# Kernel tuning notes

Measured on AMD Instinct MI355X. Metric: run time of the kernel, lower is better.

The kernel has to match this reference:

```python
import jax, jax.numpy as jnp
import numpy as np

LATENT_DIM = 128
HIDDEN = 20
BATCH = 32768


def _lstm_cell(x, h, c, W_ih, W_hh, b_ih, b_hh):
    # torch.nn.LSTMCell: gates order (i, f, g, o)
    gates = x @ W_ih.T + b_ih + h @ W_hh.T + b_hh
    i, f, g, o = jnp.split(gates, 4, axis=1)
    c_new = jax.nn.sigmoid(f) * c + jax.nn.sigmoid(i) * jnp.tanh(g)
    h_new = jax.nn.sigmoid(o) * jnp.tanh(c_new)
    return h_new, c_new


def setup_inputs() -> dict:
    key = jax.random.key(0)
    ks = jax.random.split(key, 10)
    L, H = LATENT_DIM, HIDDEN

    def u(k, shape, fan):  # torch LSTMCell init: U(-1/sqrt(hidden), 1/sqrt(hidden))
        b = 1.0 / np.sqrt(fan)
        return jax.random.uniform(k, shape, jnp.float32, -b, b)

    return {
        "mu": jax.random.normal(ks[0], (BATCH, L), jnp.float32),
        "log_var": jax.random.normal(ks[1], (BATCH, L), jnp.float32),
        "W_ih1": u(ks[2], (4 * H, L - 1), H),
        "W_hh1": u(ks[3], (4 * H, H), H),
        "b_ih1": u(ks[4], (4 * H,), H),
        "b_hh1": u(ks[5], (4 * H,), H),
        "W_ih2": u(ks[6], (8, 2 * H), 2),
        "W_hh2": u(ks[7], (8, 2), 2),
        "b_ih2": u(ks[8], (8,), 2),
        "b_hh2": u(ks[9], (8,), 2),
    }


def reference(mu, log_var, W_ih1, W_hh1, b_ih1, b_hh1, W_ih2, W_hh2, b_ih2, b_hh2):
    # sample=False path (the module's default)
    B, L = mu.shape
    H = W_hh1.shape[1]
    dt = mu.dtype
    # fixed reparameterization noise: eps[0] for the first draw, eps[k] for step k
    eps = jax.random.normal(jax.random.key(42), (L, B), dt)

    first_input = eps[0] * jnp.exp(0.5 * log_var[:, 0]) + mu[:, 0]  # [B]
    inp0 = jnp.zeros((B, L - 1), dt).at[:, 0].set(first_input)
    cols = jnp.arange(L - 1)
    mu_trunc = mu[:, : L - 1]

    def step(carry, xs):
        h1, c1, h2, c2, inp = carry
        idx, eps_t = xs
        h1, c1 = _lstm_cell(inp, h1, c1, W_ih1, W_hh1, b_ih1, b_hh1)
        out1 = jax.nn.leaky_relu(jnp.concatenate([h1, c1], axis=1))  # slope 0.01
        h2, c2 = _lstm_cell(out1, h2, c2, W_ih2, W_hh2, b_ih2, b_hh2)
        mu_r, lv_r = h2[:, 0], h2[:, 1]
        samp = eps_t * jnp.exp(0.5 * lv_r) + mu_r
        # next input = mu[:, :idx+1] zero-padded to width L-1 (sample=False branch)
        new_inp = jnp.where(cols <= idx, mu_trunc, jnp.zeros((), dt))
        return (h1, c1, h2, c2, new_inp), (mu_r, lv_r, samp)

    z = lambda n: jnp.zeros((B, n), dt)
    carry0 = (z(H), z(H), z(2), z(2), inp0)
    _, (mus, lvs, smps) = jax.lax.scan(step, carry0, (jnp.arange(1, L), eps[1:]))

    mus_full = jnp.concatenate([jnp.zeros((B, 1), dt), mus.T], axis=1)   # [B, L]
    lvs_full = jnp.concatenate([jnp.ones((B, 1), dt), lvs.T], axis=1)    # [B, L]
    samples = jnp.concatenate([first_input[:, None], smps.T], axis=1)    # [B, L]
    return mus_full, lvs_full, samples
```

## Files before the change

### kernel.cpp

```cpp
#include <hip/hip_runtime.h>
#include <stdint.h>
#include <math.h>

#define BATCH 32768
#define LDIM 128
#define HID 20

#define WS_AW  0
#define WS_AU  1280
#define WS_WCD 1792
#define WS_TOTAL 11952


__device__ __forceinline__ void threefry2x32(uint32_t x0, uint32_t x1,
                                             uint32_t& o0, uint32_t& o1) {
  const uint32_t k0 = 0u, k1 = 42u;
  const uint32_t k2 = k0 ^ k1 ^ 0x1BD11BDAu;
  uint32_t v0 = x0 + k0, v1 = x1 + k1;
#define TF_R(r) { v0 += v1; v1 = (v1 << (r)) | (v1 >> (32 - (r))); v1 ^= v0; }
  TF_R(13) TF_R(15) TF_R(26) TF_R(6)
  v0 += k1; v1 += k2 + 1u;
  TF_R(17) TF_R(29) TF_R(16) TF_R(24)
  v0 += k2; v1 += k0 + 2u;
  TF_R(13) TF_R(15) TF_R(26) TF_R(6)
  v0 += k0; v1 += k1 + 3u;
  TF_R(17) TF_R(29) TF_R(16) TF_R(24)
  v0 += k1; v1 += k2 + 4u;
  TF_R(13) TF_R(15) TF_R(26) TF_R(6)
  v0 += k2; v1 += k0 + 5u;
#undef TF_R
  o0 = v0; o1 = v1;
}

__device__ __forceinline__ float erfinv_xla_f32(float x) {
  float t = __fmul_rn(x, x);
  float w = -(float)log1p(-(double)t);
  float p;
  if (w < 5.0f) {
    w = __fadd_rn(w, -2.5f);
    p = 2.81022636e-08f;
    p = __fadd_rn(__fmul_rn(p, w), 3.43273939e-07f);
    p = __fadd_rn(__fmul_rn(p, w), -3.5233877e-06f);
    p = __fadd_rn(__fmul_rn(p, w), -4.39150654e-06f);
    p = __fadd_rn(__fmul_rn(p, w), 0.00021858087f);
    p = __fadd_rn(__fmul_rn(p, w), -0.00125372503f);
    p = __fadd_rn(__fmul_rn(p, w), -0.00417768164f);
    p = __fadd_rn(__fmul_rn(p, w), 0.246640727f);
    p = __fadd_rn(__fmul_rn(p, w), 1.50140941f);
  } else {
    w = __fadd_rn(__fsqrt_rn(w), -3.0f);
    p = -0.000200214257f;
    p = __fadd_rn(__fmul_rn(p, w), 0.000100950558f);
    p = __fadd_rn(__fmul_rn(p, w), 0.00134934322f);
    p = __fadd_rn(__fmul_rn(p, w), -0.00367342844f);
    p = __fadd_rn(__fmul_rn(p, w), 0.00573950773f);
    p = __fadd_rn(__fmul_rn(p, w), -0.0076224613f);
    p = __fadd_rn(__fmul_rn(p, w), 0.00943887047f);
    p = __fadd_rn(__fmul_rn(p, w), 1.00167406f);
    p = __fadd_rn(__fmul_rn(p, w), 2.83297682f);
  }
  return __fmul_rn(p, x);
}

__device__ __forceinline__ float eps_val(int t, int b) {
  uint32_t n = (uint32_t)t * 32768u + (uint32_t)b;
  uint32_t o0, o1;
  threefry2x32(0u, n, o0, o1);
  uint32_t bits = o0 ^ o1;
  const float lo    = __uint_as_float(0xBF7FFFFFu);
  const float sqrt2 = __uint_as_float(0x3FB504F3u);
  float f = __fadd_rn(__uint_as_float((bits >> 9) | 0x3F800000u), -1.0f);
  float u = __fadd_rn(__fmul_rn(f, 2.0f), lo);
  u = fmaxf(u, lo);
  return __fmul_rn(sqrt2, erfinv_xla_f32(u));
}

__device__ __forceinline__ float fexp2(float x) { return __builtin_amdgcn_exp2f(x); }
__device__ __forceinline__ float frcp(float x)  { return __builtin_amdgcn_rcpf(x); }
__device__ __forceinline__ float fexp(float x)  { return fexp2(1.442695040888963f * x); }
__device__ __forceinline__ float sigm(float x)  { return frcp(1.0f + fexp2(-1.442695040888963f * x)); }
__device__ __forceinline__ float tanhx(float x) { return 1.0f - 2.0f * frcp(1.0f + fexp2(2.885390081777926f * x)); }

typedef _Float16 f16x8 __attribute__((ext_vector_type(8)));
typedef _Float16 f16x2 __attribute__((ext_vector_type(2)));
typedef float    f32x4 __attribute__((ext_vector_type(4)));

__device__ __forceinline__ uint32_t packh(float x, float y) {
  f16x2 p;
  p.x = (_Float16)x;
  p.y = (_Float16)y;
  return __builtin_bit_cast(uint32_t, p);
}

__global__ void repack_kernel(const float* __restrict__ W_ih1,
                              const float* __restrict__ W_hh1,
                              const float* __restrict__ W_ih2,
                              float* __restrict__ ws) {
  uint32_t* wsu = (uint32_t*)ws;
  const int stride = gridDim.x * blockDim.x;
  const int tid0 = blockIdx.x * blockDim.x + threadIdx.x;
  for (int idx = tid0; idx < 1280; idx += stride) {
    int q = idx & 3, l = (idx >> 2) & 63, m = idx >> 8;
    int rA = l & 15, koct = l >> 4;
    int ty = rA & 3, u = 4 * m + (rA >> 2);
    int k0 = koct * 8 + 2 * q, k1 = k0 + 1;
    float w0 = (k0 < 20) ? W_hh1[(ty * 20 + u) * 20 + k0] : 0.0f;
    float w1 = (k1 < 20) ? W_hh1[(ty * 20 + u) * 20 + k1] : 0.0f;
    wsu[WS_AW + idx] = packh(w0, w1);
  }
  for (int idx = tid0; idx < 512; idx += stride) {
    int q = idx & 3, l = (idx >> 2) & 63, ks = idx >> 8;
    int j = l & 15, koct = l >> 4;
    int kk0 = ks * 32 + koct * 8 + 2 * q, kk1 = kk0 + 1;
    float w0 = (j < 8 && kk0 < 40)
                   ? W_ih2[j * 40 + (kk0 & 1) * 20 + (kk0 >> 1)] : 0.0f;
    float w1 = (j < 8 && kk1 < 40)
                   ? W_ih2[j * 40 + (kk1 & 1) * 20 + (kk1 >> 1)] : 0.0f;
    wsu[WS_AU + idx] = packh(w0, w1);
  }
  for (int idx = tid0; idx < 10160; idx += stride) {
    int grow = idx % 80, col = idx / 80;
    int u = grow >> 2, ty = grow & 3;
    ws[WS_WCD + idx] = W_ih1[(ty * 20 + u) * 127 + col];
  }
}

__global__ __launch_bounds__(256, 1) void sampler_kernel(
    const float* __restrict__ mu, const float* __restrict__ log_var,
    const float* __restrict__ ws,
    const float* __restrict__ b_ih1, const float* __restrict__ b_hh1,
    const float* __restrict__ W_hh2,
    const float* __restrict__ b_ih2, const float* __restrict__ b_hh2,
    float* __restrict__ out) {
  __shared__ float WcL[10160];
  __shared__ __align__(16) _Float16 hsh[4][640];
  __shared__ __align__(16) _Float16 lsh[4][1152];

  const int tid  = threadIdx.x;
  const int lane = tid & 63;
  const int wvl  = __builtin_amdgcn_readfirstlane(tid >> 6);
  const int sub  = lane >> 4;
  const int el   = lane & 15;
  const int elem = blockIdx.x * 64 + wvl * 16 + el;

  for (int i = tid; i < 10160; i += 256) WcL[i] = ws[WS_WCD + i];
  {
    uint32_t* hz = (uint32_t*)&hsh[0][0];
    for (int i = tid; i < 1280; i += 256) hz[i] = 0u;
    uint32_t* lz = (uint32_t*)&lsh[0][0];
    for (int i = tid; i < 2304; i += 256) lz[i] = 0u;
  }

  const uint32_t* wsu = (const uint32_t*)ws;
  f16x8 aw[5], au0, au1;
#pragma unroll
  for (int m = 0; m < 5; ++m)
    aw[m] = *(const f16x8*)(wsu + WS_AW + (m * 64 + lane) * 4);
  au0 = *(const f16x8*)(wsu + WS_AU + lane * 4);
  au1 = *(const f16x8*)(wsu + WS_AU + (64 + lane) * 4);

  __syncthreads();

  _Float16* hrow = &hsh[wvl][el * 40];
  _Float16* lrow = &lsh[wvl][el * 72];

  const float* mrow = mu + (size_t)elem * LDIM;

  float wa[4], wb[4], bb2[4], Sc[4], Ac[4], Bc[4];
#pragma unroll
  for (int r = 0; r < 4; ++r) {
    const int j = (4 * sub + r) & 7;
    wa[r]  = W_hh2[2 * j];
    wb[r]  = W_hh2[2 * j + 1];
    bb2[r] = b_ih2[j] + b_hh2[j];
    const bool isT = (j == 4) || (j == 5);
    Sc[r] = isT ?  2.885390081777926f : -1.442695040888963f;
    Ac[r] = isT ?  1.0f : 0.0f;
    Bc[r] = isT ? -2.0f : 1.0f;
  }

  float eps0 = eps_val(0, elem);
  float m0 = mrow[0];
  float fi = fmaf(eps0, fexp(0.5f * log_var[(size_t)elem * LDIM]), m0);

  f32x4 acc[5];
#pragma unroll
  for (int m = 0; m < 5; ++m) {
    f32x4 w0 = *(const f32x4*)&WcL[16 * m + 4 * sub];
#pragma unroll
    for (int r = 0; r < 4; ++r) {
      const int grow = 16 * m + 4 * sub + r;
      const int g = (grow & 3) * 20 + (grow >> 2);
      acc[m][r] = fmaf(fi, w0[r], b_ih1[g] + b_hh1[g]);
    }
  }

  float cst[5];
#pragma unroll
  for (int m = 0; m < 5; ++m) cst[m] = 0.0f;
  float h2a = 0.0f, h2b = 0.0f, c2a = 0.0f, c2b = 0.0f;

  float* out_mu = out;
  float* out_lv = out + (size_t)BATCH * LDIM;
  float* out_sp = out + 2 * (size_t)BATCH * LDIM;
  const size_t rowoff = (size_t)elem * LDIM;
  if (sub == 0)      { out_mu[rowoff] = 0.0f; out_lv[rowoff] = 1.0f; }
  else if (sub == 1) { out_sp[rowoff] = fi; }

  const f32x4 z4 = {0.0f, 0.0f, 0.0f, 0.0f};
  float xm_pref = m0;
  float eps4 = 0.0f, eps_old = 0.0f;

  auto lstm2_finish = [&](f16x8 bl0, f16x8 bl1, float eps_t, int e) {
    f32x4 d2 = __builtin_amdgcn_mfma_f32_16x16x32_f16(au0, bl0, z4, 0, 0, 0);
    d2 = __builtin_amdgcn_mfma_f32_16x16x32_f16(au1, bl1, d2, 0, 0, 0);
    float act[4];
#pragma unroll
    for (int r = 0; r < 4; ++r) {
      float g  = fmaf(h2a, wa[r], fmaf(h2b, wb[r], bb2[r])) + d2[r];
      float rc = frcp(1.0f + fexp2(Sc[r] * g));
      act[r] = fmaf(Bc[r], rc, Ac[r]);
    }
    float x0 = __shfl_xor(act[0], 16, 64);
    float x1 = __shfl_xor(act[1], 16, 64);
    float x2 = __shfl_xor(act[2], 16, 64);
    float x3 = __shfl_xor(act[3], 16, 64);
    const bool s1 = (sub & 1);
    float i20 = s1 ? x0 : act[0], i21 = s1 ? x1 : act[1];
    float f20 = s1 ? x2 : act[2], f21 = s1 ? x3 : act[3];
    float t20 = s1 ? act[0] : x0, t21 = s1 ? act[1] : x1;
    float o20 = s1 ? act[2] : x2, o21 = s1 ? act[3] : x3;
    c2a = fmaf(f20, c2a, i20 * t20);
    c2b = fmaf(f21, c2b, i21 * t21);
    h2a = o20 * tanhx(c2a);
    h2b = o21 * tanhx(c2b);
    if (sub == 0) {
      out_mu[rowoff + e] = h2a;
      out_lv[rowoff + e] = h2b;
    } else if (sub == 1) {
      out_sp[rowoff + e] = fmaf(eps_t, fexp(0.5f * h2b), h2a);
    }
  };

  for (int t = 1; t < LDIM; ++t) {
    float xm = xm_pref;
    xm_pref = mrow[t];

    const bool refresh = ((t - 1) & 3) == 0;
    if (refresh) { eps_old = eps4; eps4 = eps_val(t + sub, elem); }

    f16x8 bl0, bl1;
    if (t >= 2) {
      bl0 = *(const f16x8*)&lrow[sub * 8];
      bl1 = *(const f16x8*)&lrow[32 + sub * 8];
    }

    if (t >= 2) {
      if (t == 2) {
        float d0 = m0 - fi;
#pragma unroll
        for (int m = 0; m < 5; ++m) {
          f32x4 w0 = *(const f32x4*)&WcL[16 * m + 4 * sub];
#pragma unroll
          for (int r = 0; r < 4; ++r) acc[m][r] = fmaf(d0, w0[r], acc[m][r]);
        }
      }
#pragma unroll
      for (int m = 0; m < 5; ++m) {
        f32x4 wc = *(const f32x4*)&WcL[(t - 1) * 80 + 16 * m + 4 * sub];
#pragma unroll
        for (int r = 0; r < 4; ++r) acc[m][r] = fmaf(xm, wc[r], acc[m][r]);
      }
    }

    if (t >= 2) {
      float src = refresh ? eps_old : eps4;
      float eps_t = __shfl(src, ((t - 2) & 3) * 16 + el, 64);
      lstm2_finish(bl0, bl1, eps_t, t - 1);
    }

    f16x8 bh = *(const f16x8*)&hrow[sub * 8];
    f32x4 d[5];
#pragma unroll
    for (int m = 0; m < 5; ++m)
      d[m] = __builtin_amdgcn_mfma_f32_16x16x32_f16(aw[m], bh, acc[m], 0, 0, 0);

#pragma unroll
    for (int m = 0; m < 5; ++m) {
      float ik = sigm(d[m][0]), fk = sigm(d[m][1]);
      float gk = tanhx(d[m][2]), ok = sigm(d[m][3]);
      float cn = fmaf(fk, cst[m], ik * gk);
      cst[m] = cn;
      float hk = ok * tanhx(cn);
      hrow[4 * m + sub] = (_Float16)hk;
      float lh = (hk >= 0.0f) ? hk : 0.01f * hk;
      float lc = (cn >= 0.0f) ? cn : 0.01f * cn;
      f16x2 p; p.x = (_Float16)lh; p.y = (_Float16)lc;
      ((f16x2*)lrow)[4 * m + sub] = p;
    }
  }

  {
    f16x8 bl0 = *(const f16x8*)&lrow[sub * 8];
    f16x8 bl1 = *(const f16x8*)&lrow[32 + sub * 8];
    float eps_t = eps_val(127, elem);
    lstm2_finish(bl0, bl1, eps_t, 127);
  }
}

extern "C" void kernel_launch(void* const* d_in, const int* in_sizes, int n_in,
                              void* d_out, int out_size, void* d_ws, size_t ws_size,
                              hipStream_t stream) {
  (void)in_sizes; (void)n_in; (void)ws_size; (void)out_size;
  const float* mu      = (const float*)d_in[0];
  const float* log_var = (const float*)d_in[1];
  const float* W_ih1   = (const float*)d_in[2];
  const float* W_hh1   = (const float*)d_in[3];
  const float* b_ih1   = (const float*)d_in[4];
  const float* b_hh1   = (const float*)d_in[5];
  const float* W_ih2   = (const float*)d_in[6];
  const float* W_hh2   = (const float*)d_in[7];
  const float* b_ih2   = (const float*)d_in[8];
  const float* b_hh2   = (const float*)d_in[9];
  float* out = (float*)d_out;
  float* ws  = (float*)d_ws;

  repack_kernel<<<dim3(8), dim3(256), 0, stream>>>(W_ih1, W_hh1, W_ih2, ws);
  dim3 grid(BATCH / 64), block(256);
  sampler_kernel<<<grid, block, 0, stream>>>(mu, log_var, ws, b_ih1, b_hh1,
                                             W_hh2, b_ih2, b_hh2, out);
}
```

Baseline: 312.2 us.

## Keep MFMA B-operands in registers by permuting weight K-layout, drop LDS round-trip

```diff
diff --git a/kernel.cpp b/kernel.cpp
--- a/kernel.cpp
+++ b/kernel.cpp
@@ -84,6 +84,7 @@
 typedef _Float16 f16x8 __attribute__((ext_vector_type(8)));
 typedef _Float16 f16x2 __attribute__((ext_vector_type(2)));
 typedef float    f32x4 __attribute__((ext_vector_type(4)));
+typedef uint32_t u32x4 __attribute__((ext_vector_type(4)));
 
 __device__ __forceinline__ uint32_t packh(float x, float y) {
   f16x2 p;
@@ -104,18 +105,20 @@
     int rA = l & 15, koct = l >> 4;
     int ty = rA & 3, u = 4 * m + (rA >> 2);
     int k0 = koct * 8 + 2 * q, k1 = k0 + 1;
-    float w0 = (k0 < 20) ? W_hh1[(ty * 20 + u) * 20 + k0] : 0.0f;
-    float w1 = (k1 < 20) ? W_hh1[(ty * 20 + u) * 20 + k1] : 0.0f;
+    int mm0 = k0 & 7, mm1 = k1 & 7;
+    float w0 = (mm0 < 5) ? W_hh1[(ty * 20 + u) * 20 + (4 * mm0 + koct)] : 0.0f;
+    float w1 = (mm1 < 5) ? W_hh1[(ty * 20 + u) * 20 + (4 * mm1 + koct)] : 0.0f;
     wsu[WS_AW + idx] = packh(w0, w1);
   }
   for (int idx = tid0; idx < 512; idx += stride) {
     int q = idx & 3, l = (idx >> 2) & 63, ks = idx >> 8;
     int j = l & 15, koct = l >> 4;
-    int kk0 = ks * 32 + koct * 8 + 2 * q, kk1 = kk0 + 1;
-    float w0 = (j < 8 && kk0 < 40)
-                   ? W_ih2[j * 40 + (kk0 & 1) * 20 + (kk0 >> 1)] : 0.0f;
-    float w1 = (j < 8 && kk1 < 40)
-                   ? W_ih2[j * 40 + (kk1 & 1) * 20 + (kk1 >> 1)] : 0.0f;
+    int qq0 = 2 * q, qq1 = 2 * q + 1;
+    int mr0 = ks * 4 + (qq0 >> 1), mr1 = ks * 4 + (qq1 >> 1);
+    float w0 = (j < 8 && mr0 < 5)
+                   ? W_ih2[j * 40 + (qq0 & 1) * 20 + (4 * mr0 + koct)] : 0.0f;
+    float w1 = (j < 8 && mr1 < 5)
+                   ? W_ih2[j * 40 + (qq1 & 1) * 20 + (4 * mr1 + koct)] : 0.0f;
     wsu[WS_AU + idx] = packh(w0, w1);
   }
   for (int idx = tid0; idx < 10160; idx += stride) {
@@ -133,23 +136,14 @@
     const float* __restrict__ b_ih2, const float* __restrict__ b_hh2,
     float* __restrict__ out) {
   __shared__ float WcL[10160];
-  __shared__ __align__(16) _Float16 hsh[4][640];
-  __shared__ __align__(16) _Float16 lsh[4][1152];
 
   const int tid  = threadIdx.x;
   const int lane = tid & 63;
-  const int wvl  = __builtin_amdgcn_readfirstlane(tid >> 6);
   const int sub  = lane >> 4;
   const int el   = lane & 15;
-  const int elem = blockIdx.x * 64 + wvl * 16 + el;
+  const int elem = blockIdx.x * 64 + (tid >> 6) * 16 + el;
 
   for (int i = tid; i < 10160; i += 256) WcL[i] = ws[WS_WCD + i];
-  {
-    uint32_t* hz = (uint32_t*)&hsh[0][0];
-    for (int i = tid; i < 1280; i += 256) hz[i] = 0u;
-    uint32_t* lz = (uint32_t*)&lsh[0][0];
-    for (int i = tid; i < 2304; i += 256) lz[i] = 0u;
-  }
 
   const uint32_t* wsu = (const uint32_t*)ws;
   f16x8 aw[5], au0, au1;
@@ -160,9 +154,6 @@
   au1 = *(const f16x8*)(wsu + WS_AU + (64 + lane) * 4);
 
   __syncthreads();
-
-  _Float16* hrow = &hsh[wvl][el * 40];
-  _Float16* lrow = &lsh[wvl][el * 72];
 
   const float* mrow = mu + (size_t)elem * LDIM;
 
@@ -208,6 +199,11 @@
   else if (sub == 1) { out_sp[rowoff] = fi; }
 
   const f32x4 z4 = {0.0f, 0.0f, 0.0f, 0.0f};
+  const u32x4 zu = {0u, 0u, 0u, 0u};
+  f16x8 bh  = __builtin_bit_cast(f16x8, zu);
+  f16x8 blA = __builtin_bit_cast(f16x8, zu);
+  f16x8 blB = __builtin_bit_cast(f16x8, zu);
+
   float xm_pref = m0;
   float eps4 = 0.0f, eps_old = 0.0f;
 
@@ -249,12 +245,6 @@
     const bool refresh = ((t - 1) & 3) == 0;
     if (refresh) { eps_old = eps4; eps4 = eps_val(t + sub, elem); }
 
-    f16x8 bl0, bl1;
-    if (t >= 2) {
-      bl0 = *(const f16x8*)&lrow[sub * 8];
-      bl1 = *(const f16x8*)&lrow[32 + sub * 8];
-    }
-
     if (t >= 2) {
       if (t == 2) {
         float d0 = m0 - fi;
@@ -276,35 +266,50 @@
     if (t >= 2) {
       float src = refresh ? eps_old : eps4;
       float eps_t = __shfl(src, ((t - 2) & 3) * 16 + el, 64);
-      lstm2_finish(bl0, bl1, eps_t, t - 1);
-    }
-
-    f16x8 bh = *(const f16x8*)&hrow[sub * 8];
+      lstm2_finish(blA, blB, eps_t, t - 1);
+    }
+
     f32x4 d[5];
 #pragma unroll
     for (int m = 0; m < 5; ++m)
       d[m] = __builtin_amdgcn_mfma_f32_16x16x32_f16(aw[m], bh, acc[m], 0, 0, 0);
 
+    float hk[5], lh[5], lc[5];
 #pragma unroll
     for (int m = 0; m < 5; ++m) {
       float ik = sigm(d[m][0]), fk = sigm(d[m][1]);
       float gk = tanhx(d[m][2]), ok = sigm(d[m][3]);
       float cn = fmaf(fk, cst[m], ik * gk);
       cst[m] = cn;
-      float hk = ok * tanhx(cn);
-      hrow[4 * m + sub] = (_Float16)hk;
-      float lh = (hk >= 0.0f) ? hk : 0.01f * hk;
-      float lc = (cn >= 0.0f) ? cn : 0.01f * cn;
-      f16x2 p; p.x = (_Float16)lh; p.y = (_Float16)lc;
-      ((f16x2*)lrow)[4 * m + sub] = p;
+      float h1 = ok * tanhx(cn);
+      hk[m] = h1;
+      lh[m] = (h1 >= 0.0f) ? h1 : 0.01f * h1;
+      lc[m] = (cn >= 0.0f) ? cn : 0.01f * cn;
+    }
+
+    {
+      u32x4 tb;
+      tb.x = packh(hk[0], hk[1]);
+      tb.y = packh(hk[2], hk[3]);
+      tb.z = packh(hk[4], 0.0f);
+      tb.w = 0u;
+      bh = __builtin_bit_cast(f16x8, tb);
+      u32x4 t0;
+      t0.x = packh(lh[0], lc[0]);
+      t0.y = packh(lh[1], lc[1]);
+      t0.z = packh(lh[2], lc[2]);
+      t0.w = packh(lh[3], lc[3]);
+      blA = __builtin_bit_cast(f16x8, t0);
+      u32x4 t1;
+      t1.x = packh(lh[4], lc[4]);
+      t1.y = 0u; t1.z = 0u; t1.w = 0u;
+      blB = __builtin_bit_cast(f16x8, t1);
     }
   }
 
   {
-    f16x8 bl0 = *(const f16x8*)&lrow[sub * 8];
-    f16x8 bl1 = *(const f16x8*)&lrow[32 + sub * 8];
     float eps_t = eps_val(127, elem);
-    lstm2_finish(bl0, bl1, eps_t, 127);
+    lstm2_finish(blA, blB, eps_t, 127);
   }
 }
 
```

After: 305.2 us. 1.02x faster.
